# Optimization experiments

Hardware: AMD Instinct MI355X
Metric: run time of the kernel (lower is better)

## Reference

```python
import jax, jax.numpy as jnp
import numpy as np

N_NODES = 50000
N_EDGES = 800000
IN_FEATS = 128
HID = 64
HEADS = 3
NUM_CLASSES = 8
ATTN_SLOPE = 0.2   # DGL GATConv leaky_relu slope on attention logits
ACT_SLOPE = 0.01   # nn.LeakyReLU default


def setup_inputs() -> dict:
    key = jax.random.key(0)
    ks = jax.random.split(key, 40)
    inp = {}
    inp["x"] = jax.random.normal(ks[0], (N_NODES, IN_FEATS), dtype=jnp.float32)
    inp["src"] = jax.random.randint(ks[1], (N_EDGES,), 0, N_NODES)
    inp["dst"] = jax.random.randint(ks[2], (N_EDGES,), 0, N_NODES)
    dims_in = [IN_FEATS, HID, HID, HID, HID]
    i = 3
    for l, din in enumerate(dims_in, start=1):
        inp[f"W{l}"] = jax.random.normal(ks[i], (din, HEADS * HID), dtype=jnp.float32) / np.float32(np.sqrt(din)); i += 1
        inp[f"b{l}"] = jnp.zeros((HEADS * HID,), dtype=jnp.float32)
        inp[f"al{l}"] = jax.random.normal(ks[i], (HEADS, HID), dtype=jnp.float32) * 0.1; i += 1
        inp[f"ar{l}"] = jax.random.normal(ks[i], (HEADS, HID), dtype=jnp.float32) * 0.1; i += 1
    inp["Wo"] = jax.random.normal(ks[i], (HID, NUM_CLASSES), dtype=jnp.float32) / np.float32(np.sqrt(HID)); i += 1
    inp["bo"] = jnp.zeros((NUM_CLASSES,), dtype=jnp.float32)
    return inp


def _gatconv(h, W, b, al, ar, src, dst):
    # h: [N, din] -> feat: [N, H, F]
    feat = (h @ W).reshape(N_NODES, HEADS, HID)
    el = jnp.einsum('nhf,hf->nh', feat, al)   # [N, H]
    er = jnp.einsum('nhf,hf->nh', feat, ar)   # [N, H]
    e = jax.nn.leaky_relu(el[src] + er[dst], ATTN_SLOPE)        # [E, H]
    # numerically-stable edge softmax segmented by destination node
    m = jax.ops.segment_max(e, dst, num_segments=N_NODES)      # [N, H]
    ex = jnp.exp(e - m[dst])                                   # [E, H]
    denom = jax.ops.segment_sum(ex, dst, num_segments=N_NODES)  # [N, H]
    alpha = ex / denom[dst]                                    # [E, H]
    msg = alpha[:, :, None] * feat[src]                        # [E, H, F]
    out = jax.ops.segment_sum(msg, dst, num_segments=N_NODES)  # [N, H, F]
    return out + b.reshape(HEADS, HID)


def reference(x, src, dst,
              W1, b1, al1, ar1,
              W2, b2, al2, ar2,
              W3, b3, al3, ar3,
              W4, b4, al4, ar4,
              W5, b5, al5, ar5,
              Wo, bo):
    layers = [(W1, b1, al1, ar1), (W2, b2, al2, ar2), (W3, b3, al3, ar3),
              (W4, b4, al4, ar4), (W5, b5, al5, ar5)]
    h = x
    for (W, b, al, ar) in layers:
        h = jax.nn.leaky_relu(_gatconv(h, W, b, al, ar, src, dst), ACT_SLOPE)
        h = h.mean(axis=1)  # mean over heads -> [N, F]
    return h @ Wo + bo      # [N, num_classes]
```

## Files before the change

kernel.cpp:

```cpp
#include <hip/hip_runtime.h>
#include <hip/hip_fp16.h>
#include <cstdint>

#define N_NODES 50000
#define N_EDGES 800000
#define IN_FEATS 128
#define HID 64
#define HEADS 3
#define NUM_CLASSES 8
#define ATTN_SLOPE 0.2f
#define ACT_SLOPE 0.01f

#define NGRP 8
#define GRP_NODES 6250
#define NCHUNK 128
#define CHUNK 6250

typedef _Float16 half8 __attribute__((ext_vector_type(8)));
typedef float f32x4 __attribute__((ext_vector_type(4)));

__device__ __forceinline__ float lrelu(float x, float s) { return x > 0.f ? x : s * x; }

__global__ __launch_bounds__(256) void k_deg(const int* __restrict__ dst, int* __restrict__ deg, int E) {
    int grp = blockIdx.x & (NGRP - 1);
    int chunk = blockIdx.x >> 3;
    int lo = grp * GRP_NODES, hi = lo + GRP_NODES;
    int s = chunk * CHUNK, e = min(E, s + CHUNK);
    for (int i = s + (int)threadIdx.x; i < e; i += 256) {
        int d = dst[i];
        if (d >= lo && d < hi) atomicAdd(&deg[d], 1);
    }
}

__global__ __launch_bounds__(256) void k_scan1(const int* __restrict__ deg, int* __restrict__ off,
                                               int* __restrict__ bsum, int n) {
    __shared__ int wtot[4];
    int tid = threadIdx.x;
    int lane = tid & 63, wid = tid >> 6;
    int base = blockIdx.x * 2048 + tid * 8;
    int v[8];
    if (base + 8 <= n) {
        int4 a = *(const int4*)&deg[base];
        int4 b = *(const int4*)&deg[base + 4];
        v[0] = a.x; v[1] = a.y; v[2] = a.z; v[3] = a.w;
        v[4] = b.x; v[5] = b.y; v[6] = b.z; v[7] = b.w;
    } else {
#pragma unroll
        for (int j = 0; j < 8; ++j) v[j] = (base + j < n) ? deg[base + j] : 0;
    }
    int s[8];
    s[0] = v[0];
#pragma unroll
    for (int j = 1; j < 8; ++j) s[j] = s[j - 1] + v[j];
    int t = s[7];
    int incl = t;
    for (int o = 1; o < 64; o <<= 1) {
        int u = __shfl_up(incl, o);
        if (lane >= o) incl += u;
    }
    int excl = incl - t;
    if (lane == 63) wtot[wid] = incl;
    __syncthreads();
    int wprefix = 0;
    for (int w = 0; w < wid; ++w) wprefix += wtot[w];
    int base_off = wprefix + excl;
#pragma unroll
    for (int j = 0; j < 8; ++j)
        if (base + j < n) off[base + j] = base_off + s[j] - v[j];
    if (tid == 0) bsum[blockIdx.x] = wtot[0] + wtot[1] + wtot[2] + wtot[3];
}

__global__ __launch_bounds__(64) void k_scan2(int* __restrict__ bsum, int nb) {
    int tid = threadIdx.x;
    int v = (tid < nb) ? bsum[tid] : 0;
    int incl = v;
    for (int o = 1; o < 64; o <<= 1) {
        int u = __shfl_up(incl, o);
        if (tid >= o) incl += u;
    }
    if (tid < nb) bsum[tid] = incl - v;
}

__global__ __launch_bounds__(256) void k_scan3(int* __restrict__ off, const int* __restrict__ bsum,
                                               int n, int E) {
    int i = blockIdx.x * blockDim.x + threadIdx.x;
    if (i < n) off[i] += bsum[i >> 11];
    if (i == 0) off[n] = E;
}

__global__ __launch_bounds__(256) void k_fill(const int* __restrict__ src, const int* __restrict__ dst,
                                              const int* __restrict__ off, int* __restrict__ cur,
                                              int* __restrict__ ssrc, int E) {
    int grp = blockIdx.x & (NGRP - 1);
    int chunk = blockIdx.x >> 3;
    int lo = grp * GRP_NODES, hi = lo + GRP_NODES;
    int s = chunk * CHUNK, e = min(E, s + CHUNK);
    for (int i = s + (int)threadIdx.x; i < e; i += 256) {
        int d = dst[i];
        if (d >= lo && d < hi) {
            int p = atomicAdd(&cur[d], 1);
            ssrc[off[d] + p] = src[i];
        }
    }
}

__global__ __launch_bounds__(256) void k_xcast(const float* __restrict__ x, _Float16* __restrict__ xh, int n8) {
    int i = blockIdx.x * blockDim.x + threadIdx.x;
    if (i < n8) {
        float4 a = *(const float4*)&x[i * 8];
        float4 b = *(const float4*)&x[i * 8 + 4];
        _Float16 v[8] = {(_Float16)a.x, (_Float16)a.y, (_Float16)a.z, (_Float16)a.w,
                         (_Float16)b.x, (_Float16)b.y, (_Float16)b.z, (_Float16)b.w};
        *(uint4*)&xh[i * 8] = *(uint4*)v;
    }
}

__global__ __launch_bounds__(256) void k_wcast(const float* __restrict__ W1, const float* __restrict__ W2,
                                               const float* __restrict__ W3, const float* __restrict__ W4,
                                               const float* __restrict__ W5, _Float16* __restrict__ Wt) {
    int i = blockIdx.x * blockDim.x + threadIdx.x;
    if (i >= 24576 + 4 * 12288) return;
    const float* W; int din; int idx; _Float16* out;
    if (i < 24576) { W = W1; din = 128; idx = i; out = Wt; }
    else {
        int j = i - 24576; int l = j / 12288; idx = j % 12288;
        W = (l == 0) ? W2 : (l == 1) ? W3 : (l == 2) ? W4 : W5;
        din = 64;
        out = Wt + 24576 + l * 12288;
    }
    int col = idx / din, k = idx % din;
    out[idx] = (_Float16)W[k * 192 + col];
}

__global__ __launch_bounds__(384) void k_gemm(const _Float16* __restrict__ h, const _Float16* __restrict__ Wt,
                                              const float* __restrict__ al, const float* __restrict__ ar,
                                              _Float16* __restrict__ feat,
                                              float* __restrict__ el, float* __restrict__ er,
                                              int N, int din) {
    __shared__ __align__(16) _Float16 Hl[128 * 72];
    __shared__ __align__(16) _Float16 Wl[192 * 72];
    const int LD = 72;
    int tid = threadIdx.x;
    int row0 = blockIdx.x * 128;
    int wid = tid >> 6, lane = tid & 63;
    int head = wid >> 1, rh = wid & 1;
    int c0 = head * 64;
    int l15 = lane & 15;
    int koff = (lane >> 4) * 8;
    int wr0 = rh * 64;

    f32x4 acc[4][4] = {};

    for (int k0 = 0; k0 < din; k0 += 64) {
        if (k0 > 0) __syncthreads();
        for (int i = tid; i < 192 * 8; i += 384) {
            int col = i >> 3, c8 = i & 7;
            *(uint4*)&Wl[col * LD + c8 * 8] = *(const uint4*)&Wt[(size_t)col * din + k0 + c8 * 8];
        }
        for (int i = tid; i < 128 * 8; i += 384) {
            int r = i >> 3, c8 = i & 7;
            int row = row0 + r;
            uint4 v = make_uint4(0, 0, 0, 0);
            if (row < N) v = *(const uint4*)&h[(size_t)row * din + k0 + c8 * 8];
            *(uint4*)&Hl[r * LD + c8 * 8] = v;
        }
        __syncthreads();

#pragma unroll
        for (int kb = 0; kb < 2; ++kb) {
            int kbase = kb * 32 + koff;
            half8 b0 = *(half8*)&Wl[(c0 + l15) * LD + kbase];
            half8 b1 = *(half8*)&Wl[(c0 + 16 + l15) * LD + kbase];
            half8 b2 = *(half8*)&Wl[(c0 + 32 + l15) * LD + kbase];
            half8 b3 = *(half8*)&Wl[(c0 + 48 + l15) * LD + kbase];
#pragma unroll
            for (int rt = 0; rt < 4; ++rt) {
                half8 a = *(half8*)&Hl[(wr0 + rt * 16 + l15) * LD + kbase];
                acc[rt][0] = __builtin_amdgcn_mfma_f32_16x16x32_f16(a, b0, acc[rt][0], 0, 0, 0);
                acc[rt][1] = __builtin_amdgcn_mfma_f32_16x16x32_f16(a, b1, acc[rt][1], 0, 0, 0);
                acc[rt][2] = __builtin_amdgcn_mfma_f32_16x16x32_f16(a, b2, acc[rt][2], 0, 0, 0);
                acc[rt][3] = __builtin_amdgcn_mfma_f32_16x16x32_f16(a, b3, acc[rt][3], 0, 0, 0);
            }
        }
    }

    float alv[4], arv[4];
#pragma unroll
    for (int ct = 0; ct < 4; ++ct) {
        alv[ct] = al[c0 + ct * 16 + l15];
        arv[ct] = ar[c0 + ct * 16 + l15];
    }

#pragma unroll
    for (int rt = 0; rt < 4; ++rt) {
#pragma unroll
        for (int r = 0; r < 4; ++r) {
            int row = row0 + wr0 + rt * 16 + (lane >> 4) * 4 + r;
            bool ok = (row < N);
            float c0v = acc[rt][0][r], c1v = acc[rt][1][r], c2v = acc[rt][2][r], c3v = acc[rt][3][r];
            if (ok) {
                size_t base = (size_t)row * 192 + c0;
                feat[base + l15]      = (_Float16)c0v;
                feat[base + 16 + l15] = (_Float16)c1v;
                feat[base + 32 + l15] = (_Float16)c2v;
                feat[base + 48 + l15] = (_Float16)c3v;
            }
            float pl = c0v * alv[0] + c1v * alv[1] + c2v * alv[2] + c3v * alv[3];
            float pr = c0v * arv[0] + c1v * arv[1] + c2v * arv[2] + c3v * arv[3];
            for (int o = 1; o < 16; o <<= 1) {
                pl += __shfl_xor(pl, o);
                pr += __shfl_xor(pr, o);
            }
            if (ok && l15 == 0) {
                el[row * HEADS + head] = pl;
                er[row * HEADS + head] = pr;
            }
        }
    }
}

__global__ __launch_bounds__(64) void k_agg(const int* __restrict__ off, const int* __restrict__ ssrc,
                                            const float* __restrict__ el, const float* __restrict__ er,
                                            const __half* __restrict__ feat, const float* __restrict__ b,
                                            __half* __restrict__ hout, int N) {
    __shared__ float4 ebuf[64];
    int wid = blockIdx.x;
    int lane = threadIdx.x;
    if (wid >= N) return;
    int start = off[wid], end = off[wid + 1];
    int cnt = end - start;
    float er0 = er[wid * HEADS + 0];
    float er1 = er[wid * HEADS + 1];
    float er2 = er[wid * HEADS + 2];
    float acc0 = 0.f, acc1 = 0.f, acc2 = 0.f;
    float den0 = 0.f, den1 = 0.f, den2 = 0.f;

    if (cnt <= 64) {
        int s0 = 0;
        float ea = -3.4e38f, eb = -3.4e38f, ec = -3.4e38f;
        if (lane < cnt) {
            s0 = ssrc[start + lane];
            ea = lrelu(el[s0 * HEADS + 0] + er0, ATTN_SLOPE);
            eb = lrelu(el[s0 * HEADS + 1] + er1, ATTN_SLOPE);
            ec = lrelu(el[s0 * HEADS + 2] + er2, ATTN_SLOPE);
        }
        float ma = ea, mb = eb, mc = ec;
        for (int o = 32; o > 0; o >>= 1) {
            ma = fmaxf(ma, __shfl_xor(ma, o));
            mb = fmaxf(mb, __shfl_xor(mb, o));
            mc = fmaxf(mc, __shfl_xor(mc, o));
        }
        float xa = (lane < cnt) ? __expf(ea - ma) : 0.f;
        float xb = (lane < cnt) ? __expf(eb - mb) : 0.f;
        float xc = (lane < cnt) ? __expf(ec - mc) : 0.f;
        float da = xa, db = xb, dc = xc;
        for (int o = 32; o > 0; o >>= 1) {
            da += __shfl_xor(da, o);
            db += __shfl_xor(db, o);
            dc += __shfl_xor(dc, o);
        }
        den0 = da; den1 = db; den2 = dc;
        ebuf[lane] = make_float4(__int_as_float(s0), xa, xb, xc);
        int t = 0;
        for (; t + 4 <= cnt; t += 4) {
            float4 v0 = ebuf[t + 0];
            float4 v1 = ebuf[t + 1];
            float4 v2 = ebuf[t + 2];
            float4 v3 = ebuf[t + 3];
            const __half* f0 = feat + (size_t)__float_as_int(v0.x) * 192 + lane;
            const __half* f1 = feat + (size_t)__float_as_int(v1.x) * 192 + lane;
            const __half* f2 = feat + (size_t)__float_as_int(v2.x) * 192 + lane;
            const __half* f3 = feat + (size_t)__float_as_int(v3.x) * 192 + lane;
            float p00 = __half2float(f0[0]), p01 = __half2float(f0[64]), p02 = __half2float(f0[128]);
            float p10 = __half2float(f1[0]), p11 = __half2float(f1[64]), p12 = __half2float(f1[128]);
            float p20 = __half2float(f2[0]), p21 = __half2float(f2[64]), p22 = __half2float(f2[128]);
            float p30 = __half2float(f3[0]), p31 = __half2float(f3[64]), p32 = __half2float(f3[128]);
            acc0 += v0.y * p00; acc1 += v0.z * p01; acc2 += v0.w * p02;
            acc0 += v1.y * p10; acc1 += v1.z * p11; acc2 += v1.w * p12;
            acc0 += v2.y * p20; acc1 += v2.z * p21; acc2 += v2.w * p22;
            acc0 += v3.y * p30; acc1 += v3.z * p31; acc2 += v3.w * p32;
        }
        for (; t < cnt; ++t) {
            float4 v = ebuf[t];
            const __half* fr = feat + (size_t)__float_as_int(v.x) * 192 + lane;
            acc0 += v.y * __half2float(fr[0]);
            acc1 += v.z * __half2float(fr[64]);
            acc2 += v.w * __half2float(fr[128]);
        }
    } else {
        float ma = -3.4e38f, mb = -3.4e38f, mc = -3.4e38f;
        for (int j = start + lane; j < end; j += 64) {
            int s = ssrc[j];
            ma = fmaxf(ma, lrelu(el[s * HEADS + 0] + er0, ATTN_SLOPE));
            mb = fmaxf(mb, lrelu(el[s * HEADS + 1] + er1, ATTN_SLOPE));
            mc = fmaxf(mc, lrelu(el[s * HEADS + 2] + er2, ATTN_SLOPE));
        }
        for (int o = 32; o > 0; o >>= 1) {
            ma = fmaxf(ma, __shfl_xor(ma, o));
            mb = fmaxf(mb, __shfl_xor(mb, o));
            mc = fmaxf(mc, __shfl_xor(mc, o));
        }
        float da = 0.f, db = 0.f, dc = 0.f;
        for (int j0 = start; j0 < end; j0 += 64) {
            int jj = j0 + lane;
            int s0 = 0;
            float xa = 0.f, xb = 0.f, xc = 0.f;
            if (jj < end) {
                s0 = ssrc[jj];
                xa = __expf(lrelu(el[s0 * HEADS + 0] + er0, ATTN_SLOPE) - ma);
                xb = __expf(lrelu(el[s0 * HEADS + 1] + er1, ATTN_SLOPE) - mb);
                xc = __expf(lrelu(el[s0 * HEADS + 2] + er2, ATTN_SLOPE) - mc);
            }
            da += xa; db += xb; dc += xc;
            ebuf[lane] = make_float4(__int_as_float(s0), xa, xb, xc);
            int c = min(64, end - j0);
            int t = 0;
            for (; t + 4 <= c; t += 4) {
                float4 v0 = ebuf[t + 0];
                float4 v1 = ebuf[t + 1];
                float4 v2 = ebuf[t + 2];
                float4 v3 = ebuf[t + 3];
                const __half* f0 = feat + (size_t)__float_as_int(v0.x) * 192 + lane;
                const __half* f1 = feat + (size_t)__float_as_int(v1.x) * 192 + lane;
                const __half* f2 = feat + (size_t)__float_as_int(v2.x) * 192 + lane;
                const __half* f3 = feat + (size_t)__float_as_int(v3.x) * 192 + lane;
                float p00 = __half2float(f0[0]), p01 = __half2float(f0[64]), p02 = __half2float(f0[128]);
                float p10 = __half2float(f1[0]), p11 = __half2float(f1[64]), p12 = __half2float(f1[128]);
                float p20 = __half2float(f2[0]), p21 = __half2float(f2[64]), p22 = __half2float(f2[128]);
                float p30 = __half2float(f3[0]), p31 = __half2float(f3[64]), p32 = __half2float(f3[128]);
                acc0 += v0.y * p00; acc1 += v0.z * p01; acc2 += v0.w * p02;
                acc0 += v1.y * p10; acc1 += v1.z * p11; acc2 += v1.w * p12;
                acc0 += v2.y * p20; acc1 += v2.z * p21; acc2 += v2.w * p22;
                acc0 += v3.y * p30; acc1 += v3.z * p31; acc2 += v3.w * p32;
            }
            for (; t < c; ++t) {
                float4 v = ebuf[t];
                const __half* fr = feat + (size_t)__float_as_int(v.x) * 192 + lane;
                acc0 += v.y * __half2float(fr[0]);
                acc1 += v.z * __half2float(fr[64]);
                acc2 += v.w * __half2float(fr[128]);
            }
        }
        for (int o = 32; o > 0; o >>= 1) {
            da += __shfl_xor(da, o);
            db += __shfl_xor(db, o);
            dc += __shfl_xor(dc, o);
        }
        den0 = da; den1 = db; den2 = dc;
    }

    float v0 = (cnt > 0) ? acc0 / den0 : 0.f;
    float v1 = (cnt > 0) ? acc1 / den1 : 0.f;
    float v2 = (cnt > 0) ? acc2 / den2 : 0.f;
    float hsum = lrelu(v0 + b[lane], ACT_SLOPE)
               + lrelu(v1 + b[64 + lane], ACT_SLOPE)
               + lrelu(v2 + b[128 + lane], ACT_SLOPE);
    hout[wid * 64 + lane] = __float2half(hsum * (1.f / 3.f));
}

__global__ __launch_bounds__(256) void k_out(const __half* __restrict__ h, const float* __restrict__ Wo,
                                             const float* __restrict__ bo, float* __restrict__ out, int N) {
    __shared__ float Hl[32][65];
    __shared__ float Wl[64 * 8];
    int tid = threadIdx.x;
    int n0 = blockIdx.x * 32;
    for (int i = tid; i < 32 * 64; i += 256) {
        int r = i >> 6, k = i & 63;
        Hl[r][k] = (n0 + r < N) ? __half2float(h[(n0 + r) * 64 + k]) : 0.f;
    }
    for (int i = tid; i < 512; i += 256) Wl[i] = Wo[i];
    __syncthreads();
    int r = tid >> 3, c = tid & 7;
    float acc = 0.f;
    for (int k = 0; k < 64; ++k) acc += Hl[r][k] * Wl[k * 8 + c];
    int row = n0 + r;
    if (row < N) out[row * 8 + c] = acc + bo[c];
}

extern "C" void kernel_launch(void* const* d_in, const int* in_sizes, int n_in,
                              void* d_out, int out_size, void* d_ws, size_t ws_size,
                              hipStream_t stream) {
    const float* x  = (const float*)d_in[0];
    const int* src  = (const int*)d_in[1];
    const int* dst  = (const int*)d_in[2];
    const float *W[5], *b[5], *al[5], *ar[5];
    for (int l = 0; l < 5; ++l) {
        W[l]  = (const float*)d_in[3 + l * 4];
        b[l]  = (const float*)d_in[4 + l * 4];
        al[l] = (const float*)d_in[5 + l * 4];
        ar[l] = (const float*)d_in[6 + l * 4];
    }
    const float* Wo = (const float*)d_in[23];
    const float* bo = (const float*)d_in[24];
    float* out = (float*)d_out;

    char* ws = (char*)d_ws;
    auto alloc = [&](size_t bytes) {
        char* p = ws;
        ws += (bytes + 255) & ~size_t(255);
        return p;
    };
    _Float16* feat = (_Float16*)alloc(sizeof(_Float16) * (size_t)N_NODES * 192);
    float* el      = (float*)alloc(sizeof(float) * (size_t)N_NODES * HEADS);
    float* er      = (float*)alloc(sizeof(float) * (size_t)N_NODES * HEADS);
    _Float16* xh   = (_Float16*)alloc(sizeof(_Float16) * (size_t)N_NODES * IN_FEATS);
    _Float16* h0   = (_Float16*)alloc(sizeof(_Float16) * (size_t)N_NODES * 64);
    _Float16* h1   = (_Float16*)alloc(sizeof(_Float16) * (size_t)N_NODES * 64);
    _Float16* wt   = (_Float16*)alloc(sizeof(_Float16) * (24576 + 4 * 12288));
    int* deg    = (int*)alloc(sizeof(int) * N_NODES);
    int* off    = (int*)alloc(sizeof(int) * (N_NODES + 1));
    int* cur    = (int*)alloc(sizeof(int) * N_NODES);
    int* ssrc   = (int*)alloc(sizeof(int) * N_EDGES);
    int* bsum   = (int*)alloc(sizeof(int) * 64);

    const int NB = (N_NODES + 2047) / 2048;
    (void)hipMemsetAsync(deg, 0, sizeof(int) * N_NODES, stream);
    (void)hipMemsetAsync(cur, 0, sizeof(int) * N_NODES, stream);
    k_deg<<<NCHUNK * NGRP, 256, 0, stream>>>(dst, deg, N_EDGES);
    k_scan1<<<NB, 256, 0, stream>>>(deg, off, bsum, N_NODES);
    k_scan2<<<1, 64, 0, stream>>>(bsum, NB);
    k_scan3<<<(N_NODES + 255) / 256, 256, 0, stream>>>(off, bsum, N_NODES, N_EDGES);
    k_fill<<<NCHUNK * NGRP, 256, 0, stream>>>(src, dst, off, cur, ssrc, N_EDGES);
    k_xcast<<<(N_NODES * IN_FEATS / 8 + 255) / 256, 256, 0, stream>>>(x, xh, N_NODES * IN_FEATS / 8);
    k_wcast<<<(24576 + 4 * 12288 + 255) / 256, 256, 0, stream>>>(W[0], W[1], W[2], W[3], W[4], wt);

    const _Float16* hin = xh;
    _Float16* hbuf[2] = {h0, h1};
    const _Float16* wts[5] = {wt, wt + 24576, wt + 24576 + 12288, wt + 24576 + 2 * 12288, wt + 24576 + 3 * 12288};
    int din = IN_FEATS;
    for (int l = 0; l < 5; ++l) {
        k_gemm<<<(N_NODES + 127) / 128, 384, 0, stream>>>(hin, wts[l], al[l], ar[l], feat, el, er, N_NODES, din);
        _Float16* hn = hbuf[l & 1];
        k_agg<<<N_NODES, 64, 0, stream>>>(off, ssrc, el, er,
                                          (const __half*)feat, b[l],
                                          (__half*)hn, N_NODES);
        hin = hn;
        din = HID;
    }
    k_out<<<(N_NODES + 31) / 32, 256, 0, stream>>>((const __half*)hin, Wo, bo, out, N_NODES);
}
```

Before: 516.8 us.

## Replace LDS-tiled GEMM with single-wave blocks loading MFMA operands directly from global

The projection GEMM no longer stages H and W tiles through shared memory with 384-thread blocks. Each 64-thread block now computes a 32-row by 64-column (one head) tile and reads half8 fragments straight from global memory into MFMA operands. Barriers and LDS traffic go away and the grid gets much larger, which should help occupancy on this small-K GEMM. In exchange, inputs are re-read across the three head blocks and the global loads are strided (uncoalesced), so the kernel relies on the caches to absorb that.

```diff
diff --git a/kernel.cpp b/kernel.cpp
--- a/kernel.cpp
+++ b/kernel.cpp
@@ -132,56 +132,44 @@
     out[idx] = (_Float16)W[k * 192 + col];
 }
 
-__global__ __launch_bounds__(384) void k_gemm(const _Float16* __restrict__ h, const _Float16* __restrict__ Wt,
-                                              const float* __restrict__ al, const float* __restrict__ ar,
-                                              _Float16* __restrict__ feat,
-                                              float* __restrict__ el, float* __restrict__ er,
-                                              int N, int din) {
-    __shared__ __align__(16) _Float16 Hl[128 * 72];
-    __shared__ __align__(16) _Float16 Wl[192 * 72];
-    const int LD = 72;
-    int tid = threadIdx.x;
-    int row0 = blockIdx.x * 128;
-    int wid = tid >> 6, lane = tid & 63;
-    int head = wid >> 1, rh = wid & 1;
+__global__ __launch_bounds__(64) void k_gemm(const _Float16* __restrict__ h, const _Float16* __restrict__ Wt,
+                                             const float* __restrict__ al, const float* __restrict__ ar,
+                                             _Float16* __restrict__ feat,
+                                             float* __restrict__ el, float* __restrict__ er,
+                                             int N, int din) {
+    int bid = blockIdx.x;
+    int head = bid % 3;
+    int rt0 = bid / 3;
+    int row0 = rt0 * 32;
     int c0 = head * 64;
+    int lane = threadIdx.x;
     int l15 = lane & 15;
     int koff = (lane >> 4) * 8;
-    int wr0 = rh * 64;
-
-    f32x4 acc[4][4] = {};
-
-    for (int k0 = 0; k0 < din; k0 += 64) {
-        if (k0 > 0) __syncthreads();
-        for (int i = tid; i < 192 * 8; i += 384) {
-            int col = i >> 3, c8 = i & 7;
-            *(uint4*)&Wl[col * LD + c8 * 8] = *(const uint4*)&Wt[(size_t)col * din + k0 + c8 * 8];
-        }
-        for (int i = tid; i < 128 * 8; i += 384) {
-            int r = i >> 3, c8 = i & 7;
-            int row = row0 + r;
-            uint4 v = make_uint4(0, 0, 0, 0);
-            if (row < N) v = *(const uint4*)&h[(size_t)row * din + k0 + c8 * 8];
-            *(uint4*)&Hl[r * LD + c8 * 8] = v;
-        }
-        __syncthreads();
-
-#pragma unroll
-        for (int kb = 0; kb < 2; ++kb) {
-            int kbase = kb * 32 + koff;
-            half8 b0 = *(half8*)&Wl[(c0 + l15) * LD + kbase];
-            half8 b1 = *(half8*)&Wl[(c0 + 16 + l15) * LD + kbase];
-            half8 b2 = *(half8*)&Wl[(c0 + 32 + l15) * LD + kbase];
-            half8 b3 = *(half8*)&Wl[(c0 + 48 + l15) * LD + kbase];
-#pragma unroll
-            for (int rt = 0; rt < 4; ++rt) {
-                half8 a = *(half8*)&Hl[(wr0 + rt * 16 + l15) * LD + kbase];
-                acc[rt][0] = __builtin_amdgcn_mfma_f32_16x16x32_f16(a, b0, acc[rt][0], 0, 0, 0);
-                acc[rt][1] = __builtin_amdgcn_mfma_f32_16x16x32_f16(a, b1, acc[rt][1], 0, 0, 0);
-                acc[rt][2] = __builtin_amdgcn_mfma_f32_16x16x32_f16(a, b2, acc[rt][2], 0, 0, 0);
-                acc[rt][3] = __builtin_amdgcn_mfma_f32_16x16x32_f16(a, b3, acc[rt][3], 0, 0, 0);
-            }
-        }
+
+    f32x4 acc[2][4] = {};
+    int r0 = min(row0 + l15, N - 1);
+    int r1 = min(row0 + 16 + l15, N - 1);
+    const _Float16* wbase = Wt + (size_t)(c0 + l15) * din + koff;
+    const _Float16* hbase0 = h + (size_t)r0 * din + koff;
+    const _Float16* hbase1 = h + (size_t)r1 * din + koff;
+
+    int nkb = din >> 5;
+    for (int kb = 0; kb < nkb; ++kb) {
+        int kb32 = kb * 32;
+        half8 b0 = *(const half8*)&wbase[kb32];
+        half8 b1 = *(const half8*)&wbase[16 * din + kb32];
+        half8 b2 = *(const half8*)&wbase[32 * din + kb32];
+        half8 b3 = *(const half8*)&wbase[48 * din + kb32];
+        half8 a0 = *(const half8*)&hbase0[kb32];
+        half8 a1 = *(const half8*)&hbase1[kb32];
+        acc[0][0] = __builtin_amdgcn_mfma_f32_16x16x32_f16(a0, b0, acc[0][0], 0, 0, 0);
+        acc[0][1] = __builtin_amdgcn_mfma_f32_16x16x32_f16(a0, b1, acc[0][1], 0, 0, 0);
+        acc[0][2] = __builtin_amdgcn_mfma_f32_16x16x32_f16(a0, b2, acc[0][2], 0, 0, 0);
+        acc[0][3] = __builtin_amdgcn_mfma_f32_16x16x32_f16(a0, b3, acc[0][3], 0, 0, 0);
+        acc[1][0] = __builtin_amdgcn_mfma_f32_16x16x32_f16(a1, b0, acc[1][0], 0, 0, 0);
+        acc[1][1] = __builtin_amdgcn_mfma_f32_16x16x32_f16(a1, b1, acc[1][1], 0, 0, 0);
+        acc[1][2] = __builtin_amdgcn_mfma_f32_16x16x32_f16(a1, b2, acc[1][2], 0, 0, 0);
+        acc[1][3] = __builtin_amdgcn_mfma_f32_16x16x32_f16(a1, b3, acc[1][3], 0, 0, 0);
     }
 
     float alv[4], arv[4];
@@ -192,10 +180,10 @@
     }
 
 #pragma unroll
-    for (int rt = 0; rt < 4; ++rt) {
+    for (int rt = 0; rt < 2; ++rt) {
 #pragma unroll
         for (int r = 0; r < 4; ++r) {
-            int row = row0 + wr0 + rt * 16 + (lane >> 4) * 4 + r;
+            int row = row0 + rt * 16 + (lane >> 4) * 4 + r;
             bool ok = (row < N);
             float c0v = acc[rt][0][r], c1v = acc[rt][1][r], c2v = acc[rt][2][r], c3v = acc[rt][3][r];
             if (ok) {
@@ -429,7 +417,8 @@
     const _Float16* wts[5] = {wt, wt + 24576, wt + 24576 + 12288, wt + 24576 + 2 * 12288, wt + 24576 + 3 * 12288};
     int din = IN_FEATS;
     for (int l = 0; l < 5; ++l) {
-        k_gemm<<<(N_NODES + 127) / 128, 384, 0, stream>>>(hin, wts[l], al[l], ar[l], feat, el, er, N_NODES, din);
+        int nrt = (N_NODES + 31) / 32;
+        k_gemm<<<nrt * 3, 64, 0, stream>>>(hin, wts[l], al[l], ar[l], feat, el, er, N_NODES, din);
         _Float16* hn = hbuf[l & 1];
         k_agg<<<N_NODES, 64, 0, stream>>>(off, ssrc, el, er,
                                           (const __half*)feat, b[l],
```

Measured after the change: 514.4 us. About the same (-0.5%).
